# Optimization experiments

Hardware: AMD Instinct MI355X
Metric: run time of the kernel (lower is better)

The kernel has to match this reference:

```python
import jax, jax.numpy as jnp
import numpy as np

D_MODEL = 1024
N_HEAD = 16


def setup_inputs() -> dict:
    key = jax.random.key(0)
    ks = jax.random.split(key, 12)
    B, S, D = 4, 2048, D_MODEL
    scale = 1.0 / np.sqrt(D)
    inp = {
        "Q": jax.random.normal(ks[0], (B, S, D), jnp.float32),
        "K": jax.random.normal(ks[1], (B, S, D), jnp.float32),
        "V": jax.random.normal(ks[2], (B, S, D), jnp.float32),
        "Wq": jax.random.normal(ks[3], (D, D), jnp.float32) * scale,
        "bq": jax.random.normal(ks[4], (D,), jnp.float32) * scale,
        "Wk": jax.random.normal(ks[5], (D, D), jnp.float32) * scale,
        "bk": jax.random.normal(ks[6], (D,), jnp.float32) * scale,
        "Wv": jax.random.normal(ks[7], (D, D), jnp.float32) * scale,
        "bv": jax.random.normal(ks[8], (D,), jnp.float32) * scale,
        "Wo": jax.random.normal(ks[9], (D, D), jnp.float32) * scale,
        "bo": jax.random.normal(ks[10], (D,), jnp.float32) * scale,
    }
    return inp


def _split_heads(x, n_head):
    B, S, D = x.shape
    return x.reshape(B, S, n_head, D // n_head).transpose(0, 2, 1, 3)  # [B,H,S,dh]


def reference(Q, K, V, Wq, bq, Wk, bk, Wv, bv, Wo, bo):
    # torch Linear: x @ W.T + b
    q = _split_heads(Q @ Wq.T + bq, N_HEAD)
    k = _split_heads(K @ Wk.T + bk, N_HEAD)
    v = _split_heads(V @ Wv.T + bv, N_HEAD)
    d_k = k.shape[-1]
    score = jnp.einsum('bhqd,bhkd->bhqk', q, k) / jnp.sqrt(jnp.float32(d_k))
    attn = jax.nn.softmax(score, axis=-1)
    out = jnp.einsum('bhqk,bhkd->bhqd', attn, v)  # [B,H,S,dh]
    B, H, S, dh = out.shape
    out = out.transpose(0, 2, 1, 3).reshape(B, S, H * dh)
    return out @ Wo.T + bo
```

## Files before the change

### kernel.cpp

```cpp
#include <hip/hip_runtime.h>
#include <math.h>

#define D_MODEL 1024
#define N_HEAD  16
#define DH      64
#define SEQ     2048
#define BATCH   4
#define BH      (BATCH*N_HEAD)
#define MROWS   (BATCH*SEQ)

typedef __attribute__((ext_vector_type(8)))  short          s16x8;
typedef __attribute__((ext_vector_type(8)))  unsigned short u16x8;
typedef __attribute__((ext_vector_type(4)))  unsigned short u16x4;
typedef __attribute__((ext_vector_type(4)))  float          f32x4;
typedef __attribute__((ext_vector_type(16))) float          f32x16;
typedef __attribute__((ext_vector_type(4)))  unsigned int   u32x4;

#define QSCALE 0.18033688f

typedef const __attribute__((address_space(1))) unsigned int gu32;
typedef __attribute__((address_space(3))) unsigned int lu32;
#define GLOAD_LDS16(g, l) __builtin_amdgcn_global_load_lds((gu32*)(g), (lu32*)(l), 16, 0, 0)

__device__ __forceinline__ unsigned short f2bf(float x) {
    unsigned int u = __float_as_uint(x);
    u += 0x7FFFu + ((u >> 16) & 1u);
    return (unsigned short)(u >> 16);
}

__device__ __forceinline__ unsigned int cvtpk_bf16(float lo, float hi) {
    unsigned int r;
    asm("v_cvt_pk_bf16_f32 %0, %1, %2" : "=v"(r) : "v"(lo), "v"(hi));
    return r;
}

__device__ __forceinline__ float exp2_asm(float x) {
    float r;
    asm("v_exp_f32 %0, %1" : "=v"(r) : "v"(x));
    return r;
}

__device__ __forceinline__ float max3f(float a, float b, float c) {
    float r;
    asm("v_max3_f32 %0, %1, %2, %3" : "=v"(r) : "v"(a), "v"(b), "v"(c));
    return r;
}

__global__ __launch_bounds__(256) void conv_w4(const float* __restrict__ w0,
                                               const float* __restrict__ w1,
                                               const float* __restrict__ w2,
                                               const float* __restrict__ w3,
                                               unsigned short* __restrict__ o0,
                                               unsigned short* __restrict__ o1,
                                               unsigned short* __restrict__ o2,
                                               unsigned short* __restrict__ o3)
{
    const float* w; unsigned short* o;
    switch (blockIdx.y) {
        case 0:  w = w0; o = o0; break;
        case 1:  w = w1; o = o1; break;
        case 2:  w = w2; o = o2; break;
        default: w = w3; o = o3; break;
    }
    int i = blockIdx.x * 256 + threadIdx.x;
    const float4* p = (const float4*)w + (size_t)i * 2;
    float4 a = p[0], b = p[1];
    u16x8 v;
    v[0] = f2bf(a.x); v[1] = f2bf(a.y); v[2] = f2bf(a.z); v[3] = f2bf(a.w);
    v[4] = f2bf(b.x); v[5] = f2bf(b.y); v[6] = f2bf(b.z); v[7] = f2bf(b.w);
    *((u16x8*)o + i) = v;
}

template<int MODE, bool AF32>
__global__ __launch_bounds__(256) void gemm_bt(const void* __restrict__ Av,
                                               const unsigned short* __restrict__ W,
                                               const float* __restrict__ bias,
                                               unsigned short* __restrict__ outb,
                                               float* __restrict__ outf,
                                               float oscale)
{
    __shared__ short As[2][128 * 64];
    __shared__ short Bs[2][128 * 64];
    const int tid = threadIdx.x;
    const int w = tid >> 6, l = tid & 63;
    const int lr = l & 15, lg = l >> 4;
    const int wm = w >> 1, wn = w & 1;
    const int r0 = blockIdx.x * 128, c0 = blockIdx.y * 128;
    const int srow = tid >> 3;
    const int sc8  = tid & 7;

    f32x4 zz = {0.f, 0.f, 0.f, 0.f};
    f32x4 acc[4][4];
    #pragma unroll
    for (int i = 0; i < 4; ++i)
        #pragma unroll
        for (int j = 0; j < 4; ++j) acc[i][j] = zz;

    const unsigned short* Ab = (const unsigned short*)Av;
    const float*          Af = (const float*)Av;

    const int lrow8 = l >> 3;
    const int lslot = l & 7;
    size_t bsrc[4];
    #pragma unroll
    for (int p = 0; p < 4; ++p)
        bsrc[p] = ((size_t)(c0 + w * 32 + p * 8 + lrow8) * 1024 + (size_t)((lslot ^ lrow8) * 8)) * 2;

    u16x8 ar[2][4];
    float4 arf[2][4][2];
    #pragma unroll
    for (int sub = 0; sub < 2; ++sub) {
        #pragma unroll
        for (int p = 0; p < 4; ++p) {
            int row = p * 32 + srow;
            if (AF32) {
                arf[sub][p][0] = *(const float4*)(Af + (size_t)(r0 + row) * 1024 + sub * 64 + sc8 * 8);
                arf[sub][p][1] = *(const float4*)(Af + (size_t)(r0 + row) * 1024 + sub * 64 + sc8 * 8 + 4);
            } else {
                ar[sub][p] = *(const u16x8*)(Ab + (size_t)(r0 + row) * 1024 + sub * 64 + sc8 * 8);
            }
        }
    }

    for (int ks = 0; ks < 8; ++ks) {
        __syncthreads();
        #pragma unroll
        for (int sub = 0; sub < 2; ++sub)
            #pragma unroll
            for (int p = 0; p < 4; ++p)
                GLOAD_LDS16((const char*)W + bsrc[p] + (size_t)ks * 256 + sub * 128,
                            &Bs[sub][(w * 32 + p * 8) * 64]);
        #pragma unroll
        for (int sub = 0; sub < 2; ++sub) {
            #pragma unroll
            for (int p = 0; p < 4; ++p) {
                int row = p * 32 + srow;
                if (AF32) {
                    u32x4 wd;
                    wd[0] = cvtpk_bf16(arf[sub][p][0].x, arf[sub][p][0].y);
                    wd[1] = cvtpk_bf16(arf[sub][p][0].z, arf[sub][p][0].w);
                    wd[2] = cvtpk_bf16(arf[sub][p][1].x, arf[sub][p][1].y);
                    wd[3] = cvtpk_bf16(arf[sub][p][1].z, arf[sub][p][1].w);
                    *(u16x8*)&As[sub][row * 64 + ((sc8 ^ (row & 7)) * 8)] = __builtin_bit_cast(u16x8, wd);
                } else {
                    *(u16x8*)&As[sub][row * 64 + ((sc8 ^ (row & 7)) * 8)] = ar[sub][p];
                }
            }
        }
        __syncthreads();
        if (ks < 7) {
            int k0 = (ks + 1) * 128;
            #pragma unroll
            for (int sub = 0; sub < 2; ++sub) {
                #pragma unroll
                for (int p = 0; p < 4; ++p) {
                    int row = p * 32 + srow;
                    if (AF32) {
                        arf[sub][p][0] = *(const float4*)(Af + (size_t)(r0 + row) * 1024 + k0 + sub * 64 + sc8 * 8);
                        arf[sub][p][1] = *(const float4*)(Af + (size_t)(r0 + row) * 1024 + k0 + sub * 64 + sc8 * 8 + 4);
                    } else {
                        ar[sub][p] = *(const u16x8*)(Ab + (size_t)(r0 + row) * 1024 + k0 + sub * 64 + sc8 * 8);
                    }
                }
            }
        }
        #pragma unroll
        for (int sub = 0; sub < 2; ++sub) {
            #pragma unroll
            for (int t = 0; t < 2; ++t) {
                const int k8 = lg + 4 * t;
                s16x8 af[4], bw[4];
                #pragma unroll
                for (int i = 0; i < 4; ++i) {
                    int rowa = wm * 64 + i * 16 + lr;
                    af[i] = *(const s16x8*)&As[sub][rowa * 64 + ((k8 ^ (rowa & 7)) * 8)];
                    int rowb = wn * 64 + i * 16 + lr;
                    bw[i] = *(const s16x8*)&Bs[sub][rowb * 64 + ((k8 ^ (rowb & 7)) * 8)];
                }
                #pragma unroll
                for (int i = 0; i < 4; ++i)
                    #pragma unroll
                    for (int j = 0; j < 4; ++j)
                        acc[i][j] = __builtin_amdgcn_mfma_f32_16x16x32_bf16(af[i], bw[j], acc[i][j], 0, 0, 0);
            }
        }
    }

    #pragma unroll
    for (int i = 0; i < 4; ++i) {
        #pragma unroll
        for (int j = 0; j < 4; ++j) {
            const int colb = c0 + wn * 64 + j * 16 + lr;
            const float bv = bias[colb];
            if (MODE == 2) {
                const int row = r0 + wm * 64 + i * 16 + lg * 4;
                const int b = row >> 11, s = row & 2047;
                const int h = colb >> 6, d = colb & 63;
                u16x4 pv;
                pv[0] = f2bf((acc[i][j][0] + bv) * oscale);
                pv[1] = f2bf((acc[i][j][1] + bv) * oscale);
                pv[2] = f2bf((acc[i][j][2] + bv) * oscale);
                pv[3] = f2bf((acc[i][j][3] + bv) * oscale);
                *(u16x4*)(outb + ((size_t)(b * N_HEAD + h) * DH + d) * SEQ + s) = pv;
            } else {
                #pragma unroll
                for (int rg = 0; rg < 4; ++rg) {
                    const int row = r0 + wm * 64 + i * 16 + lg * 4 + rg;
                    const float v = acc[i][j][rg] + bv;
                    if (MODE == 0) {
                        outf[(size_t)row * D_MODEL + colb] = v;
                    } else {
                        const int b = row >> 11, s = row & 2047;
                        const int h = colb >> 6, d = colb & 63;
                        outb[((size_t)(b * N_HEAD + h) * SEQ + s) * DH + d] = f2bf(v * oscale);
                    }
                }
            }
        }
    }
}

__global__ __launch_bounds__(256, 4) void flash_attn_mfma32(const unsigned short* __restrict__ qb,
                                                            const unsigned short* __restrict__ kb,
                                                            const unsigned short* __restrict__ vtb,
                                                            unsigned short* __restrict__ aob)
{
    __shared__ u16x8 Kt[2][512];
    __shared__ u16x8 Vt[2][512];

    const int tid = threadIdx.x;
    const int w = tid >> 6, l = tid & 63;
    const int q32 = l & 31;
    const int h = l >> 5;

    const int wg   = blockIdx.x;
    const int xcd  = wg & 7;
    const int slot = wg >> 3;
    const int bh   = xcd * 8 + (slot >> 4);
    const int qt   = slot & 15;

    const unsigned short* qh = qb + (size_t)bh * SEQ * DH;
    const unsigned short* kh = kb + (size_t)bh * SEQ * DH;
    const unsigned short* vh = vtb + (size_t)bh * DH * SEQ;

    const int qrow = qt * 128 + w * 32 + q32;

    s16x8 qf[4];
    #pragma unroll
    for (int ks = 0; ks < 4; ++ks)
        qf[ks] = *(const s16x8*)(qh + (size_t)qrow * DH + ks * 16 + h * 8);

    f32x16 O[2];
    #pragma unroll
    for (int r = 0; r < 16; ++r) { O[0][r] = 0.f; O[1][r] = 0.f; }
    float m = 0.f, lsum = 0.f;

    const int srow = tid >> 3;
    const int sc8  = tid & 7;

    u16x8 kreg[2], vreg[2];
    #pragma unroll
    for (int p = 0; p < 2; ++p) {
        int rr = p * 32 + srow;
        kreg[p] = *(const u16x8*)(kh + (size_t)rr * DH + sc8 * 8);
        vreg[p] = *(const u16x8*)(vh + (size_t)rr * SEQ + sc8 * 8);
    }
    #pragma unroll
    for (int p = 0; p < 2; ++p) {
        int rr = p * 32 + srow;
        Kt[0][sc8 * 64 + (rr ^ sc8)] = kreg[p];
        Vt[0][sc8 * 64 + (rr ^ sc8)] = vreg[p];
    }
    __syncthreads();

    int buf = 0;
    for (int kv = 0; kv < SEQ / 64; ++kv) {
        if (kv < SEQ / 64 - 1) {
            const int s0 = (kv + 1) * 64;
            #pragma unroll
            for (int p = 0; p < 2; ++p) {
                int rr = p * 32 + srow;
                kreg[p] = *(const u16x8*)(kh + (size_t)(s0 + rr) * DH + sc8 * 8);
                vreg[p] = *(const u16x8*)(vh + (size_t)rr * SEQ + s0 + sc8 * 8);
            }
        }

        f32x16 SC[2];
        #pragma unroll
        for (int r = 0; r < 16; ++r) { SC[0][r] = -m; SC[1][r] = -m; }
        __builtin_amdgcn_s_setprio(1);
        #pragma unroll
        for (int ks = 0; ks < 4; ++ks) {
            const int chunk = 2 * ks + h;
            #pragma unroll
            for (int c = 0; c < 2; ++c) {
                const int row = c * 32 + q32;
                s16x8 kf = __builtin_bit_cast(s16x8, Kt[buf][chunk * 64 + (row ^ chunk)]);
                SC[c] = __builtin_amdgcn_mfma_f32_32x32x16_bf16(kf, qf[ks], SC[c], 0, 0, 0);
            }
        }
        __builtin_amdgcn_s_setprio(0);

        #define GETSC(i) ((i) < 16 ? SC[0][(i)] : SC[1][(i) - 16])
        float t0[11];
        #pragma unroll
        for (int r = 0; r < 10; ++r)
            t0[r] = max3f(GETSC(3 * r), GETSC(3 * r + 1), GETSC(3 * r + 2));
        t0[10] = fmaxf(GETSC(30), GETSC(31));
        float u0 = max3f(t0[0], t0[1], t0[2]);
        float u1 = max3f(t0[3], t0[4], t0[5]);
        float u2 = max3f(t0[6], t0[7], t0[8]);
        float u3 = fmaxf(t0[9], t0[10]);
        float rmb_l = fmaxf(max3f(u0, u1, u2), u3);
        float rmb = fmaxf(rmb_l, __shfl_xor(rmb_l, 32, 64));
        #undef GETSC

        if (!__all(rmb <= 8.0f)) {
            const float delta = fmaxf(rmb, 0.f);
            const float fold = exp2_asm(-delta);
            lsum *= fold;
            O[0] *= fold;
            O[1] *= fold;
            m += delta;
            #pragma unroll
            for (int c = 0; c < 2; ++c)
                #pragma unroll
                for (int r = 0; r < 16; ++r)
                    SC[c][r] -= delta;
        }

        #pragma unroll
        for (int c = 0; c < 2; ++c)
            #pragma unroll
            for (int r = 0; r < 16; ++r)
                SC[c][r] = exp2_asm(SC[c][r]);

        float s0a[8];
        #pragma unroll
        for (int r = 0; r < 8; ++r)
            s0a[r] = (SC[0][r] + SC[0][r + 8]) + (SC[1][r] + SC[1][r + 8]);
        #pragma unroll
        for (int d = 4; d; d >>= 1)
            #pragma unroll
            for (int r = 0; r < d; ++r) s0a[r] += s0a[r + d];
        lsum += s0a[0] + __shfl_xor(s0a[0], 32, 64);

        s16x8 pa[4];
        #pragma unroll
        for (int s = 0; s < 4; ++s) {
            const int c = s >> 1, rb = (s & 1) * 8;
            unsigned int a0 = cvtpk_bf16(SC[c][rb + 0], SC[c][rb + 1]);
            unsigned int a1 = cvtpk_bf16(SC[c][rb + 2], SC[c][rb + 3]);
            unsigned int b0 = cvtpk_bf16(SC[c][rb + 4], SC[c][rb + 5]);
            unsigned int b1 = cvtpk_bf16(SC[c][rb + 6], SC[c][rb + 7]);
            asm volatile("v_permlane32_swap_b32 %0, %1" : "+v"(a0), "+v"(b0));
            asm volatile("v_permlane32_swap_b32 %0, %1" : "+v"(a1), "+v"(b1));
            u32x4 wd;
            wd[0] = a0;
            wd[1] = a1;
            wd[2] = b0;
            wd[3] = b1;
            pa[s] = __builtin_bit_cast(s16x8, wd);
        }

        __builtin_amdgcn_s_setprio(1);
        #pragma unroll
        for (int s = 0; s < 4; ++s) {
            const int chunk = 2 * s + h;
            #pragma unroll
            for (int c = 0; c < 2; ++c) {
                const int row = c * 32 + q32;
                s16x8 vf = __builtin_bit_cast(s16x8, Vt[buf][chunk * 64 + (row ^ chunk)]);
                O[c] = __builtin_amdgcn_mfma_f32_32x32x16_bf16(vf, pa[s], O[c], 0, 0, 0);
            }
        }
        __builtin_amdgcn_s_setprio(0);

        if (kv < SEQ / 64 - 1) {
            #pragma unroll
            for (int p = 0; p < 2; ++p) {
                int rr = p * 32 + srow;
                Kt[buf ^ 1][sc8 * 64 + (rr ^ sc8)] = kreg[p];
                Vt[buf ^ 1][sc8 * 64 + (rr ^ sc8)] = vreg[p];
            }
            __syncthreads();
            buf ^= 1;
        }
    }

    const float inv = 1.0f / lsum;
    const int b = bh >> 4, head = bh & 15;
    unsigned short* obase = aob + ((size_t)b * SEQ + qrow) * D_MODEL + head * DH;
    #pragma unroll
    for (int c = 0; c < 2; ++c) {
        #pragma unroll
        for (int rq = 0; rq < 4; ++rq) {
            const int d0 = 8 * rq + 4 * h + 32 * c;
            u16x4 pv;
            #pragma unroll
            for (int j = 0; j < 4; ++j) pv[j] = f2bf(O[c][rq * 4 + j] * inv);
            *(u16x4*)(obase + d0) = pv;
        }
    }
}

extern "C" void kernel_launch(void* const* d_in, const int* in_sizes, int n_in,
                              void* d_out, int out_size, void* d_ws, size_t ws_size,
                              hipStream_t stream)
{
    const float* Q  = (const float*)d_in[0];
    const float* K  = (const float*)d_in[1];
    const float* V  = (const float*)d_in[2];
    const float* Wq = (const float*)d_in[3];
    const float* bq = (const float*)d_in[4];
    const float* Wk = (const float*)d_in[5];
    const float* bk = (const float*)d_in[6];
    const float* Wv = (const float*)d_in[7];
    const float* bv = (const float*)d_in[8];
    const float* Wo = (const float*)d_in[9];
    const float* bo = (const float*)d_in[10];

    const size_t PER = (size_t)MROWS * D_MODEL;
    const size_t WSZ = (size_t)D_MODEL * D_MODEL;
    unsigned short* wqb = (unsigned short*)d_ws;
    unsigned short* wkb = wqb + WSZ;
    unsigned short* wvb = wkb + WSZ;
    unsigned short* wob = wvb + WSZ;
    unsigned short* qb2 = wob + WSZ;
    unsigned short* kb2 = qb2 + PER;
    unsigned short* vtb = kb2 + PER;
    unsigned short* aob = vtb + PER;

    dim3 gg(MROWS / 128, D_MODEL / 128);

    conv_w4<<<dim3(512, 4), 256, 0, stream>>>(Wq, Wk, Wv, Wo, wqb, wkb, wvb, wob);

    gemm_bt<1, true><<<gg, 256, 0, stream>>>(Q, wqb, bq, qb2, nullptr, QSCALE);
    gemm_bt<1, true><<<gg, 256, 0, stream>>>(K, wkb, bk, kb2, nullptr, 1.0f);
    gemm_bt<2, true><<<gg, 256, 0, stream>>>(V, wvb, bv, vtb, nullptr, 1.0f);

    flash_attn_mfma32<<<dim3(16 * BH), 256, 0, stream>>>(qb2, kb2, vtb, aob);

    gemm_bt<0, false><<<gg, 256, 0, stream>>>(aob, wob, bo, nullptr, (float*)d_out, 1.0f);
}
```

Measured before the change: 212.2 us.

## Software-pipeline attention: overlap next tile's QK^T with current softmax and PV

```diff
diff --git a/kernel.cpp b/kernel.cpp
--- a/kernel.cpp
+++ b/kernel.cpp
@@ -220,13 +220,13 @@
     }
 }
 
-__global__ __launch_bounds__(256, 4) void flash_attn_mfma32(const unsigned short* __restrict__ qb,
+__global__ __launch_bounds__(256, 3) void flash_attn_mfma32(const unsigned short* __restrict__ qb,
                                                             const unsigned short* __restrict__ kb,
                                                             const unsigned short* __restrict__ vtb,
                                                             unsigned short* __restrict__ aob)
 {
-    __shared__ u16x8 Kt[2][512];
-    __shared__ u16x8 Vt[2][512];
+    __shared__ u16x8 Kt[3][512];
+    __shared__ u16x8 Vt[3][512];
 
     const int tid = threadIdx.x;
     const int w = tid >> 6, l = tid & 63;
@@ -250,7 +250,7 @@
     for (int ks = 0; ks < 4; ++ks)
         qf[ks] = *(const s16x8*)(qh + (size_t)qrow * DH + ks * 16 + h * 8);
 
-    f32x16 O[2];
+    f32x16 O[2], SA[2], SB[2];
     #pragma unroll
     for (int r = 0; r < 16; ++r) { O[0][r] = 0.f; O[1][r] = 0.f; }
     float m = 0.f, lsum = 0.f;
@@ -273,120 +273,150 @@
     }
     __syncthreads();
 
-    int buf = 0;
-    for (int kv = 0; kv < SEQ / 64; ++kv) {
-        if (kv < SEQ / 64 - 1) {
-            const int s0 = (kv + 1) * 64;
-            #pragma unroll
-            for (int p = 0; p < 2; ++p) {
-                int rr = p * 32 + srow;
-                kreg[p] = *(const u16x8*)(kh + (size_t)(s0 + rr) * DH + sc8 * 8);
-                vreg[p] = *(const u16x8*)(vh + (size_t)rr * SEQ + s0 + sc8 * 8);
-            }
-        }
-
-        f32x16 SC[2];
-        #pragma unroll
-        for (int r = 0; r < 16; ++r) { SC[0][r] = -m; SC[1][r] = -m; }
-        __builtin_amdgcn_s_setprio(1);
-        #pragma unroll
-        for (int ks = 0; ks < 4; ++ks) {
-            const int chunk = 2 * ks + h;
-            #pragma unroll
-            for (int c = 0; c < 2; ++c) {
-                const int row = c * 32 + q32;
-                s16x8 kf = __builtin_bit_cast(s16x8, Kt[buf][chunk * 64 + (row ^ chunk)]);
-                SC[c] = __builtin_amdgcn_mfma_f32_32x32x16_bf16(kf, qf[ks], SC[c], 0, 0, 0);
-            }
-        }
-        __builtin_amdgcn_s_setprio(0);
-
-        #define GETSC(i) ((i) < 16 ? SC[0][(i)] : SC[1][(i) - 16])
-        float t0[11];
-        #pragma unroll
-        for (int r = 0; r < 10; ++r)
-            t0[r] = max3f(GETSC(3 * r), GETSC(3 * r + 1), GETSC(3 * r + 2));
-        t0[10] = fmaxf(GETSC(30), GETSC(31));
-        float u0 = max3f(t0[0], t0[1], t0[2]);
-        float u1 = max3f(t0[3], t0[4], t0[5]);
-        float u2 = max3f(t0[6], t0[7], t0[8]);
-        float u3 = fmaxf(t0[9], t0[10]);
-        float rmb_l = fmaxf(max3f(u0, u1, u2), u3);
-        float rmb = fmaxf(rmb_l, __shfl_xor(rmb_l, 32, 64));
-        #undef GETSC
-
-        if (!__all(rmb <= 8.0f)) {
-            const float delta = fmaxf(rmb, 0.f);
-            const float fold = exp2_asm(-delta);
-            lsum *= fold;
-            O[0] *= fold;
-            O[1] *= fold;
-            m += delta;
-            #pragma unroll
-            for (int c = 0; c < 2; ++c)
-                #pragma unroll
-                for (int r = 0; r < 16; ++r)
-                    SC[c][r] -= delta;
-        }
-
-        #pragma unroll
-        for (int c = 0; c < 2; ++c)
-            #pragma unroll
-            for (int r = 0; r < 16; ++r)
-                SC[c][r] = exp2_asm(SC[c][r]);
-
-        float s0a[8];
-        #pragma unroll
-        for (int r = 0; r < 8; ++r)
-            s0a[r] = (SC[0][r] + SC[0][r + 8]) + (SC[1][r] + SC[1][r + 8]);
-        #pragma unroll
-        for (int d = 4; d; d >>= 1)
-            #pragma unroll
-            for (int r = 0; r < d; ++r) s0a[r] += s0a[r + d];
-        lsum += s0a[0] + __shfl_xor(s0a[0], 32, 64);
-
-        s16x8 pa[4];
-        #pragma unroll
-        for (int s = 0; s < 4; ++s) {
-            const int c = s >> 1, rb = (s & 1) * 8;
-            unsigned int a0 = cvtpk_bf16(SC[c][rb + 0], SC[c][rb + 1]);
-            unsigned int a1 = cvtpk_bf16(SC[c][rb + 2], SC[c][rb + 3]);
-            unsigned int b0 = cvtpk_bf16(SC[c][rb + 4], SC[c][rb + 5]);
-            unsigned int b1 = cvtpk_bf16(SC[c][rb + 6], SC[c][rb + 7]);
-            asm volatile("v_permlane32_swap_b32 %0, %1" : "+v"(a0), "+v"(b0));
-            asm volatile("v_permlane32_swap_b32 %0, %1" : "+v"(a1), "+v"(b1));
-            u32x4 wd;
-            wd[0] = a0;
-            wd[1] = a1;
-            wd[2] = b0;
-            wd[3] = b1;
-            pa[s] = __builtin_bit_cast(s16x8, wd);
-        }
-
-        __builtin_amdgcn_s_setprio(1);
-        #pragma unroll
-        for (int s = 0; s < 4; ++s) {
-            const int chunk = 2 * s + h;
-            #pragma unroll
-            for (int c = 0; c < 2; ++c) {
-                const int row = c * 32 + q32;
-                s16x8 vf = __builtin_bit_cast(s16x8, Vt[buf][chunk * 64 + (row ^ chunk)]);
-                O[c] = __builtin_amdgcn_mfma_f32_32x32x16_bf16(vf, pa[s], O[c], 0, 0, 0);
-            }
-        }
-        __builtin_amdgcn_s_setprio(0);
-
-        if (kv < SEQ / 64 - 1) {
-            #pragma unroll
-            for (int p = 0; p < 2; ++p) {
-                int rr = p * 32 + srow;
-                Kt[buf ^ 1][sc8 * 64 + (rr ^ sc8)] = kreg[p];
-                Vt[buf ^ 1][sc8 * 64 + (rr ^ sc8)] = vreg[p];
-            }
-            __syncthreads();
-            buf ^= 1;
-        }
-    }
+#define FA_QK(CUR, SLQ)                                                          \
+    {                                                                            \
+        _Pragma("unroll")                                                        \
+        for (int r_ = 0; r_ < 16; ++r_) { CUR[0][r_] = 0.f; CUR[1][r_] = 0.f; }  \
+        __builtin_amdgcn_s_setprio(1);                                           \
+        _Pragma("unroll")                                                        \
+        for (int ks_ = 0; ks_ < 4; ++ks_) {                                      \
+            const int chunk_ = 2 * ks_ + h;                                      \
+            _Pragma("unroll")                                                    \
+            for (int c_ = 0; c_ < 2; ++c_) {                                     \
+                const int row_ = c_ * 32 + q32;                                  \
+                s16x8 kf_ = __builtin_bit_cast(s16x8, Kt[SLQ][chunk_ * 64 + (row_ ^ chunk_)]); \
+                CUR[c_] = __builtin_amdgcn_mfma_f32_32x32x16_bf16(kf_, qf[ks_], CUR[c_], 0, 0, 0); \
+            }                                                                    \
+        }                                                                        \
+        __builtin_amdgcn_s_setprio(0);                                           \
+    }
+
+#define FA_SMPV(PRV, VSL)                                                        \
+    {                                                                            \
+        float t0_[11];                                                           \
+        _Pragma("unroll")                                                        \
+        for (int r_ = 0; r_ < 10; ++r_) {                                        \
+            float a_ = (3*r_   < 16) ? PRV[0][3*r_  ] : PRV[1][3*r_-16];         \
+            float b_ = (3*r_+1 < 16) ? PRV[0][3*r_+1] : PRV[1][3*r_-15];         \
+            float c_ = (3*r_+2 < 16) ? PRV[0][3*r_+2] : PRV[1][3*r_-14];         \
+            t0_[r_] = max3f(a_, b_, c_);                                         \
+        }                                                                        \
+        t0_[10] = fmaxf(PRV[1][14], PRV[1][15]);                                 \
+        float u0_ = max3f(t0_[0], t0_[1], t0_[2]);                               \
+        float u1_ = max3f(t0_[3], t0_[4], t0_[5]);                               \
+        float u2_ = max3f(t0_[6], t0_[7], t0_[8]);                               \
+        float u3_ = fmaxf(t0_[9], t0_[10]);                                      \
+        float rmb_l_ = fmaxf(max3f(u0_, u1_, u2_), u3_);                         \
+        float rmb_ = fmaxf(rmb_l_, __shfl_xor(rmb_l_, 32, 64));                  \
+        if (!__all(rmb_ - m <= 8.0f)) {                                          \
+            const float delta_ = fmaxf(rmb_ - m, 0.f);                           \
+            const float fold_ = exp2_asm(-delta_);                               \
+            lsum *= fold_;                                                       \
+            O[0] *= fold_;                                                       \
+            O[1] *= fold_;                                                       \
+            m += delta_;                                                         \
+        }                                                                        \
+        _Pragma("unroll")                                                        \
+        for (int c_ = 0; c_ < 2; ++c_)                                           \
+            _Pragma("unroll")                                                    \
+            for (int r_ = 0; r_ < 16; ++r_)                                      \
+                PRV[c_][r_] = exp2_asm(PRV[c_][r_] - m);                         \
+        s16x8 pa_[4];                                                            \
+        _Pragma("unroll")                                                        \
+        for (int s_ = 0; s_ < 4; ++s_) {                                         \
+            const int c_ = s_ >> 1, rb_ = (s_ & 1) * 8;                          \
+            unsigned int a0_ = cvtpk_bf16(PRV[c_][rb_ + 0], PRV[c_][rb_ + 1]);   \
+            unsigned int a1_ = cvtpk_bf16(PRV[c_][rb_ + 2], PRV[c_][rb_ + 3]);   \
+            unsigned int b0_ = cvtpk_bf16(PRV[c_][rb_ + 4], PRV[c_][rb_ + 5]);   \
+            unsigned int b1_ = cvtpk_bf16(PRV[c_][rb_ + 6], PRV[c_][rb_ + 7]);   \
+            asm volatile("v_permlane32_swap_b32 %0, %1" : "+v"(a0_), "+v"(b0_)); \
+            asm volatile("v_permlane32_swap_b32 %0, %1" : "+v"(a1_), "+v"(b1_)); \
+            u32x4 wd_;                                                           \
+            wd_[0] = a0_; wd_[1] = a1_; wd_[2] = b0_; wd_[3] = b1_;              \
+            pa_[s_] = __builtin_bit_cast(s16x8, wd_);                            \
+        }                                                                        \
+        __builtin_amdgcn_s_setprio(1);                                           \
+        _Pragma("unroll")                                                        \
+        for (int s_ = 0; s_ < 4; ++s_) {                                         \
+            const int chunk_ = 2 * s_ + h;                                       \
+            _Pragma("unroll")                                                    \
+            for (int c_ = 0; c_ < 2; ++c_) {                                     \
+                const int row_ = c_ * 32 + q32;                                  \
+                s16x8 vf_ = __builtin_bit_cast(s16x8, Vt[VSL][chunk_ * 64 + (row_ ^ chunk_)]); \
+                O[c_] = __builtin_amdgcn_mfma_f32_32x32x16_bf16(vf_, pa_[s_], O[c_], 0, 0, 0); \
+            }                                                                    \
+        }                                                                        \
+        __builtin_amdgcn_s_setprio(0);                                           \
+        float s0a_[8];                                                           \
+        _Pragma("unroll")                                                        \
+        for (int r_ = 0; r_ < 8; ++r_)                                           \
+            s0a_[r_] = (PRV[0][r_] + PRV[0][r_ + 8]) + (PRV[1][r_] + PRV[1][r_ + 8]); \
+        _Pragma("unroll")                                                        \
+        for (int d_ = 4; d_; d_ >>= 1)                                           \
+            _Pragma("unroll")                                                    \
+            for (int r_ = 0; r_ < d_; ++r_) s0a_[r_] += s0a_[r_ + d_];           \
+        lsum += s0a_[0] + __shfl_xor(s0a_[0], 32, 64);                           \
+    }
+
+#define FA_PREF(I1)                                                              \
+    {                                                                            \
+        const int s0_ = (I1) * 64;                                               \
+        _Pragma("unroll")                                                        \
+        for (int p_ = 0; p_ < 2; ++p_) {                                         \
+            int rr_ = p_ * 32 + srow;                                            \
+            kreg[p_] = *(const u16x8*)(kh + (size_t)(s0_ + rr_) * DH + sc8 * 8); \
+            vreg[p_] = *(const u16x8*)(vh + (size_t)rr_ * SEQ + s0_ + sc8 * 8);  \
+        }                                                                        \
+    }
+
+#define FA_STAGE(SLN)                                                            \
+    {                                                                            \
+        _Pragma("unroll")                                                        \
+        for (int p_ = 0; p_ < 2; ++p_) {                                         \
+            int rr_ = p_ * 32 + srow;                                            \
+            Kt[SLN][sc8 * 64 + (rr_ ^ sc8)] = kreg[p_];                          \
+            Vt[SLN][sc8 * 64 + (rr_ ^ sc8)] = vreg[p_];                          \
+        }                                                                        \
+        __syncthreads();                                                         \
+    }
+
+    int slq = 0;
+    {
+        FA_PREF(1);
+        FA_QK(SA, 0);
+        FA_STAGE(1);
+        slq = 1;
+    }
+    for (int base = 1; base < 31; base += 2) {
+        {
+            const int i_ = base;
+            FA_PREF(i_ + 1);
+            FA_QK(SB, slq);
+            const int slp = (slq + 2) % 3;
+            FA_SMPV(SA, slp);
+            const int sln = slq + 1 == 3 ? 0 : slq + 1;
+            FA_STAGE(sln);
+            slq = sln;
+        }
+        {
+            const int i_ = base + 1;
+            if (i_ < 31) FA_PREF(i_ + 1);
+            FA_QK(SA, slq);
+            const int slp = (slq + 2) % 3;
+            FA_SMPV(SB, slp);
+            if (i_ < 31) {
+                const int sln = slq + 1 == 3 ? 0 : slq + 1;
+                FA_STAGE(sln);
+                slq = sln;
+            }
+        }
+    }
+    {
+        FA_QK(SB, slq);
+        const int slp = (slq + 2) % 3;
+        FA_SMPV(SA, slp);
+    }
+    FA_SMPV(SB, slq);
 
     const float inv = 1.0f / lsum;
     const int b = bh >> 4, head = bh & 15;
@@ -402,6 +432,10 @@
             *(u16x4*)(obase + d0) = pv;
         }
     }
+#undef FA_QK
+#undef FA_SMPV
+#undef FA_PREF
+#undef FA_STAGE
 }
 
 extern "C" void kernel_launch(void* const* d_in, const int* in_sizes, int n_in,
```

Result: slower. 239.9 us (+13.1%).
